# Optimization experiments

Measured on AMD Instinct MI355X. Metric: run time of the kernel, lower is better.

The kernel has to match this reference:

```python
import jax, jax.numpy as jnp
import numpy as np

# Loihi neuron constants (from netParams['neuron'])
VTH_MANT = 80.0
THETA = VTH_MANT * 64.0          # Loihi threshold = vThMant * 2**6
I_DECAY = 1024.0                 # current decay (of 4096)
V_DECAY = 128.0                  # voltage decay (of 4096)
REF_DELAY = 1.0                  # refractory steps after a spike
W_SCALE = 64.0                   # Loihi weighted-input scaling (2**6)
TAU_RHO = 1.0
POOL_W = 1.1 * VTH_MANT          # slayer pool synapse weight (one spike fires output)


@jax.custom_vjp
def spike(v):
    return (v >= THETA).astype(v.dtype)

def _spike_fwd(v):
    return spike(v), v

def _spike_bwd(v, g):
    # SLAYER surrogate gradient: exponential pdf around threshold
    return (g * jnp.exp(-jnp.abs(v - THETA) / (TAU_RHO * THETA)) / THETA,)

spike.defvjp(_spike_fwd, _spike_bwd)


def loihi_dynamics(wsum):
    """CUBA Loihi LIF over time-leading weighted input wsum: [T, ...] -> spikes [T, ...]."""
    i_dec = (4096.0 - I_DECAY) / 4096.0
    v_dec = (4096.0 - V_DECAY) / 4096.0

    def step(carry, x):
        u, v, ref = carry
        u = i_dec * u + W_SCALE * x                    # synaptic current
        v = jnp.where(ref > 0, 0.0, v_dec * v + u)     # membrane, clamped in refractory
        s = spike(v)
        v = v * (1.0 - s)                              # reset on spike
        ref = jnp.where(s > 0, REF_DELAY, jnp.maximum(ref - 1.0, 0.0))
        return (u, v, ref), s

    z = jnp.zeros_like(wsum[0])
    _, s = jax.lax.scan(step, (z, z, z), wsum)
    return s


def delay_shift(s):
    # slayer.delayShift(spike, 1): shift spike train by 1 timestep (time-leading axis)
    return jnp.concatenate([jnp.zeros_like(s[:1]), s[:-1]], axis=0)


def conv2d_t(x, w, pad):
    # x: [T, B, C, H, W]; fold T into batch for the spatial conv
    T, B, C, H, W = x.shape
    y = jax.lax.conv_general_dilated(
        x.reshape(T * B, C, H, W), w, (1, 1), [(pad, pad), (pad, pad)],
        dimension_numbers=('NCHW', 'OIHW', 'NCHW'))
    return y.reshape(T, B, y.shape[1], y.shape[2], y.shape[3])


def sum_pool(x, k):
    # slayer pool: per-channel sum pooling with fixed synaptic weight POOL_W
    y = jax.lax.reduce_window(x, 0.0, jax.lax.add,
                              (1, 1, 1, k, k), (1, 1, 1, k, k), 'VALID')
    return POOL_W * y


def setup_inputs() -> dict:
    key = jax.random.key(0)
    ks = jax.random.split(key, 6)
    B, C, H, W, T = 48, 4, 26, 26, 128
    # Bernoulli(0.1) spike trains
    spike_input = (jax.random.uniform(ks[0], (B, C, H, W, T)) < 0.1).astype(jnp.float32)
    w_conv1 = jax.random.normal(ks[1], (8, 4, 5, 5), jnp.float32) * 4.0
    w_conv2 = jax.random.normal(ks[2], (16, 8, 3, 3), jnp.float32) * 4.0
    w_conv3 = jax.random.normal(ks[3], (32, 16, 3, 3), jnp.float32) * 4.0
    w_fc1 = jax.random.normal(ks[4], (512, 3 * 3 * 32), jnp.float32) * 4.0
    w_fc2 = jax.random.normal(ks[5], (2, 512), jnp.float32) * 4.0
    return {"spike_input": spike_input, "w_conv1": w_conv1, "w_conv2": w_conv2,
            "w_conv3": w_conv3, "w_fc1": w_fc1, "w_fc2": w_fc2}


def reference(spike_input, w_conv1, w_conv2, w_conv3, w_fc1, w_fc2):
    x = jnp.transpose(spike_input, (4, 0, 1, 2, 3))  # [T, B, C, H, W]

    def block(x, w, pad):
        s = delay_shift(loihi_dynamics(conv2d_t(x, w, pad)))
        s = delay_shift(loihi_dynamics(sum_pool(s, 2)))
        return s  # dropout is identity in eval

    x = block(x, w_conv1, 1)   # 26 -> 24 -> 12
    x = block(x, w_conv2, 1)   # 12 -> 12 -> 6
    x = block(x, w_conv3, 1)   # 6 -> 6 -> 3
    T, B = x.shape[0], x.shape[1]
    x = x.reshape(T, B, -1)    # [T, B, 32*3*3] (C,H,W flatten order matches torch view)
    s = delay_shift(loihi_dynamics(jnp.einsum('tbi,oi->tbo', x, w_fc1)))
    s = delay_shift(loihi_dynamics(jnp.einsum('tbi,oi->tbo', s, w_fc2)))
    return jnp.transpose(s, (1, 2, 0))  # [B, 2, T]
```

## Files before the change

### kernel.cpp

```cpp
#include <hip/hip_runtime.h>


#define THETA 5120.0f

typedef __attribute__((ext_vector_type(8))) short bfrag;
typedef __attribute__((ext_vector_type(4))) float ffrag;

__device__ __forceinline__ float dyn_step(float x, float& u, float& v, float& r) {
#pragma clang fp contract(off)
    u = 0.75f * u + 64.0f * x;
    float vn = 0.96875f * v + u;
    vn = (r > 0.0f) ? 0.0f : vn;
    float s;
    if (vn >= THETA) { s = 1.0f; v = 0.0f; r = 1.0f; }
    else             { s = 0.0f; v = vn; r = fmaxf(r - 1.0f, 0.0f); }
    return s;
}

__device__ __forceinline__ float dpp_add_xor1(float x) {
    int y = __builtin_amdgcn_update_dpp(0, __float_as_int(x), 0xB1, 0xF, 0xF, true);
    return x + __int_as_float(y);
}
__device__ __forceinline__ float dpp_add_xor2(float x) {
    int y = __builtin_amdgcn_update_dpp(0, __float_as_int(x), 0x4E, 0xF, 0xF, true);
    return x + __int_as_float(y);
}

__device__ __forceinline__ unsigned int compress4(unsigned long long x) {
    x &= 0x1111111111111111ull;
    x = (x | (x >> 3))  & 0x0303030303030303ull;
    x = (x | (x >> 6))  & 0x000F000F000F000Full;
    x = (x | (x >> 12)) & 0x000000FF000000FFull;
    x = (x | (x >> 24)) & 0xFFFFull;
    return (unsigned int)x;
}

__device__ __forceinline__ unsigned short f2bf(float f) {
    unsigned int u = __float_as_uint(f);
    unsigned int r = (u + 0x7FFFu + ((u >> 16) & 1u)) >> 16;
    return (unsigned short)r;
}
__device__ __forceinline__ float bf2f(unsigned short b) {
    return __uint_as_float(((unsigned int)b) << 16);
}

__device__ __forceinline__ float f4_elem(float4 v, int j) {
    return (j == 0) ? v.x : (j == 1) ? v.y : (j == 2) ? v.z : v.w;
}

__global__ __launch_bounds__(256) void k_masks(const float* __restrict__ in,
                                               const float* __restrict__ wfc1,
                                               uint2* __restrict__ xb,
                                               unsigned short* __restrict__ wb) {
    if (blockIdx.x >= 624) {
        int gid = (blockIdx.x - 624) * 256 + threadIdx.x;
        int o = gid / 288, k = gid % 288;
        float w = wfc1[gid];
        unsigned short b0 = f2bf(w);
        float r1 = w - bf2f(b0);
        unsigned short b1 = f2bf(r1);
        float r2 = r1 - bf2f(b1);
        unsigned short b2 = f2bf(r2);
        size_t ob = (size_t)o * 864 + k;
        wb[ob]       = b0;
        wb[ob + 288] = b1;
        wb[ob + 576] = b2;
        return;
    }
    int wv = blockIdx.x * 4 + (threadIdx.x >> 6);
    int lane = threadIdx.x & 63;
    int y = wv % 26; int r = wv / 26;
    int pr = r & 1; int b = r >> 1;
    int ch = lane >> 5;
    int x = lane & 31;
    int act = x < 26;
    int xc = act ? x : 25;
    const float4* src = (const float4*)(in + (size_t)(((b * 4 + pr * 2 + ch) * 26 + y) * 26 + xc) * 128);
    uint2* dst = xb + ((size_t)b * 2 + pr) * 28 + (y + 1);
    if (y == 0) {
        uint2* pp = xb + ((size_t)b * 2 + pr) * 28;
        uint2 z = make_uint2(0u, 0u);
#pragma unroll
        for (int h = 0; h < 2; ++h) {
            int t = h * 64 + lane;
            pp[(size_t)t * 2688] = z;
            pp[(size_t)t * 2688 + 27] = z;
        }
    }
    for (int t4 = 0; t4 < 32; ++t4) {
        float4 f = src[t4];
#pragma unroll
        for (int k = 0; k < 4; ++k) {
            float fv = f4_elem(f, k);
            unsigned long long bal = __ballot(act && (fv != 0.0f));
            if (lane == 0) {
                unsigned int lo = ((unsigned int)bal & 0x03FFFFFFu) << 1;
                unsigned int hi = ((unsigned int)(bal >> 32) & 0x03FFFFFFu) << 1;
                dst[(size_t)(t4 * 4 + k) * 2688] = make_uint2(lo, hi);
            }
        }
    }
}

__global__ __launch_bounds__(576) void k_wsum1(const uint2* __restrict__ xb,
                                               const float* __restrict__ w1,
                                               float* __restrict__ ws) {
    __shared__ float wsh[400];
    __shared__ ffrag tbl4[660];
    int tid = threadIdx.x;
    int H = blockIdx.x & 1;
    int bid = blockIdx.x >> 1;
    int tch = bid & 15;
    int b = bid >> 4;
    float* wsH = ws + (size_t)H * 14155776;
    if (tid < 400) wsh[tid] = w1[H * 400 + tid];
    __syncthreads();
    for (int e = tid; e < 660; e += 576) {
        int ch = e / 165;
        int rem = e % 165;
        int ky = rem / 33;
        int idx = rem % 33;
        ffrag val = {0.f, 0.f, 0.f, 0.f};
#pragma unroll
        for (int oc4 = 0; oc4 < 4; ++oc4) {
            float a = 0.f;
#pragma unroll
            for (int k = 0; k < 5; ++k)
                a += ((idx >> k) & 1) ? wsh[oc4 * 100 + ch * 25 + ky * 5 + k] : 0.f;
            val[oc4] = a;
        }
        tbl4[(ch * 5 + ky) * 33 + idx] = val;
    }
    __syncthreads();
    int q = tid >> 2, s = tid & 3;
    int ox = (q % 12) * 2 + (s & 1);
    int oy = (q / 12) * 2 + (s >> 1);
    int t0 = tch * 8;
    ffrag acc[8];
#pragma unroll
    for (int j = 0; j < 8; ++j) {
        int t = t0 + j;
        const uint2* rp = xb + ((size_t)t * 48 + b) * 56 + oy;
        ffrag a = {0.f, 0.f, 0.f, 0.f};
#pragma unroll
        for (int ky = 0; ky < 5; ++ky) {
            uint2 r0 = rp[ky];
            uint2 r1 = rp[28 + ky];
            a += tbl4[ky * 33 + (int)((r0.x >> ox) & 31u)];
            a += tbl4[(5 + ky) * 33 + (int)((r0.y >> ox) & 31u)];
            a += tbl4[(10 + ky) * 33 + (int)((r1.x >> ox) & 31u)];
            a += tbl4[(15 + ky) * 33 + (int)((r1.y >> ox) & 31u)];
        }
        acc[j] = a;
    }
    size_t tilebase = (size_t)(t0 >> 4) * 1769472 + (t0 & 15);
#pragma unroll
    for (int oc4 = 0; oc4 < 4; ++oc4) {
        float* wp = wsH + tilebase + (size_t)((b * 4 + oc4) * 576 + tid) * 16;
        *(float4*)(wp)     = make_float4(acc[0][oc4], acc[1][oc4], acc[2][oc4], acc[3][oc4]);
        *(float4*)(wp + 4) = make_float4(acc[4][oc4], acc[5][oc4], acc[6][oc4], acc[7][oc4]);
    }
}

__global__ __launch_bounds__(576) void k_scan1(const float* __restrict__ ws,
                                               unsigned short* __restrict__ pb16) {
    __shared__ unsigned short sh[9 * 128];
    int tid = threadIdx.x;
    int sub = tid >> 6, lane = tid & 63;
    int blk = blockIdx.x;
    int H = (blk >= 192) ? 1 : 0;
    int ibl = blk - H * 192;
    int b = ibl >> 2, ocl = ibl & 3;
    int oc = H * 4 + ocl;
    const float* bp = ws + (size_t)H * 14155776 + (size_t)((ibl * 9 + sub) * 64 + lane) * 16;
    float u = 0.f, v = 0.f, rf = 0.f;
    float pu = 0.f, pv = 0.f, prf = 0.f;
    float sp = 0.f;
    unsigned int mb[4];
    float4 cur[4], nxt[4];
#pragma unroll
    for (int i = 0; i < 4; ++i) cur[i] = *(const float4*)(bp + i * 4);
    for (int tb = 0; tb < 8; ++tb) {
        if (tb < 7) {
            const float* np = bp + (size_t)(tb + 1) * 1769472;
#pragma unroll
            for (int i = 0; i < 4; ++i) nxt[i] = *(const float4*)(np + i * 4);
        }
#pragma unroll
        for (int j = 0; j < 16; ++j) {
            int t = tb * 16 + j;
            float w = f4_elem(cur[j >> 2], j & 3);
            float cnt = dpp_add_xor2(dpp_add_xor1(sp));
            float ps = dyn_step(88.0f * cnt, pu, pv, prf);
            unsigned long long bal = __ballot(((lane & 3) == 0) && (ps > 0.5f));
            unsigned int m = compress4(bal);
            int sl = (t >> 1) & 3;
            mb[sl] = (t & 1) ? (mb[sl] | (m << 16)) : m;
            if ((t & 7) == 7 && lane == 0)
                *(uint4*)(&sh[sub * 128 + (t & ~7)]) = make_uint4(mb[0], mb[1], mb[2], mb[3]);
            sp = dyn_step(w, u, v, rf);
        }
        if (tb < 7) {
#pragma unroll
            for (int i = 0; i < 4; ++i) cur[i] = nxt[i];
        }
    }
    __syncthreads();
    for (int idx = tid; idx < 1536; idx += 576) {
        int t = idx / 12, y = idx % 12;
        int Q0 = y * 12;
        int w0 = Q0 >> 4, off = Q0 & 15;
        unsigned int v0 = sh[w0 * 128 + t];
        unsigned int v1 = (off > 4) ? (unsigned int)sh[(w0 + 1) * 128 + t] : 0u;
        unsigned int m = ((v0 >> off) | (v1 << (16 - off))) & 0xFFFu;
        size_t rowb = (size_t)(t * 48 + b) * 14;
        pb16[(rowb + y + 1) * 8 + oc] = (unsigned short)(m << 1);
        if (y == 0)  pb16[rowb * 8 + oc] = 0;
        if (y == 11) pb16[(rowb + 13) * 8 + oc] = 0;
    }
}

__global__ __launch_bounds__(576) void k_wsum2(const unsigned short* __restrict__ pb16,
                                               const float* __restrict__ w2,
                                               float* __restrict__ ws) {
    __shared__ float wsh[288];
    __shared__ ffrag tbl4[852];
    int tid = threadIdx.x;
    int tch = blockIdx.x & 3;
    int r = blockIdx.x >> 2;
    int ocg = r & 3; int b = r >> 2;
    if (tid < 288) wsh[tid] = w2[(ocg * 4 + tid / 72) * 72 + (tid % 72)];
    __syncthreads();
    for (int e = tid; e < 852; e += 576) {
        int pr = e / 213;
        int rem = e % 213;
        int ky = rem / 71;
        int idx = rem % 71;
        int lo = idx % 9, hi = idx / 9;
        ffrag val = {0.f, 0.f, 0.f, 0.f};
#pragma unroll
        for (int oc4 = 0; oc4 < 4; ++oc4) {
            float a = 0.f;
#pragma unroll
            for (int k = 0; k < 3; ++k)
                a += ((lo >> k) & 1) ? wsh[oc4 * 72 + (2 * pr) * 9 + ky * 3 + k] : 0.f;
#pragma unroll
            for (int k = 0; k < 3; ++k)
                a += ((hi >> k) & 1) ? wsh[oc4 * 72 + (2 * pr + 1) * 9 + ky * 3 + k] : 0.f;
            val[oc4] = a;
        }
        tbl4[(pr * 3 + ky) * 71 + idx] = val;
    }
    __syncthreads();
    int tq = tid / 144;
    int pix = tid % 144;
    int q = pix >> 2, s = pix & 3;
    int ox = (q % 6) * 2 + (s & 1);
    int oy = (q / 6) * 2 + (s >> 1);
    int t0 = tch * 32 + tq * 8;
    ffrag acc[8];
#pragma unroll
    for (int j = 0; j < 8; ++j) {
        int t = t0 + j;
        ffrag a = {0.f, 0.f, 0.f, 0.f};
        if (t > 0) {
            const uint4* rp = (const uint4*)(pb16 + (((size_t)(t - 1) * 48 + b) * 14 + oy) * 8);
#pragma unroll
            for (int ky = 0; ky < 3; ++ky) {
                uint4 row = rp[ky];
                unsigned int wd[4] = {row.x, row.y, row.z, row.w};
#pragma unroll
                for (int pr = 0; pr < 4; ++pr) {
                    unsigned int lo = (wd[pr] >> ox) & 7u;
                    unsigned int hi = (wd[pr] >> (16 + ox)) & 7u;
                    a += tbl4[(pr * 3 + ky) * 71 + (int)(lo + 9u * hi)];
                }
            }
        }
        acc[j] = a;
    }
    size_t tilebase = (size_t)(t0 >> 4) * 1769472 + (t0 & 15);
#pragma unroll
    for (int oc4 = 0; oc4 < 4; ++oc4) {
        int neuron = (b * 16 + ocg * 4 + oc4) * 144 + pix;
        float* wp = ws + tilebase + (size_t)neuron * 16;
        *(float4*)(wp)     = make_float4(acc[0][oc4], acc[1][oc4], acc[2][oc4], acc[3][oc4]);
        *(float4*)(wp + 4) = make_float4(acc[4][oc4], acc[5][oc4], acc[6][oc4], acc[7][oc4]);
    }
}

__global__ __launch_bounds__(576) void k_scan2(const float* __restrict__ ws,
                                               unsigned short* __restrict__ pb2) {
    __shared__ unsigned short sh[9 * 128];
    int tid = threadIdx.x;
    int wloc = tid >> 6, lane = tid & 63;
    int g4 = blockIdx.x;
    const float* bp = ws + (size_t)(g4 * 576 + tid) * 16;
    float u = 0.f, v = 0.f, rf = 0.f;
    float pu = 0.f, pv = 0.f, prf = 0.f;
    float sp = 0.f;
    unsigned int mb[4];
    float4 cur[4], nxt[4];
#pragma unroll
    for (int i = 0; i < 4; ++i) cur[i] = *(const float4*)(bp + i * 4);
    for (int tb = 0; tb < 8; ++tb) {
        if (tb < 7) {
            const float* np = bp + (size_t)(tb + 1) * 1769472;
#pragma unroll
            for (int i = 0; i < 4; ++i) nxt[i] = *(const float4*)(np + i * 4);
        }
#pragma unroll
        for (int j = 0; j < 16; ++j) {
            int t = tb * 16 + j;
            float w = f4_elem(cur[j >> 2], j & 3);
            float cnt = dpp_add_xor2(dpp_add_xor1(sp));
            float ps = dyn_step(88.0f * cnt, pu, pv, prf);
            unsigned long long bal = __ballot(((lane & 3) == 0) && (ps > 0.5f));
            unsigned int m = compress4(bal);
            int sl = (t >> 1) & 3;
            mb[sl] = (t & 1) ? (mb[sl] | (m << 16)) : m;
            if ((t & 7) == 7 && lane == 0)
                *(uint4*)(&sh[wloc * 128 + (t & ~7)]) = make_uint4(mb[0], mb[1], mb[2], mb[3]);
            sp = dyn_step(w, u, v, rf);
        }
        if (tb < 7) {
#pragma unroll
            for (int i = 0; i < 4; ++i) cur[i] = nxt[i];
        }
    }
    __syncthreads();
    for (int idx = tid; idx < 3072; idx += 576) {
        int t = idx / 24;
        int r2 = idx % 24;
        int lI = r2 / 6, y = r2 % 6;
        int img = g4 * 4 + lI;
        int b = img >> 4, oc = img & 15;
        int Q0 = lI * 36 + y * 6;
        int w0 = Q0 >> 4, off = Q0 & 15;
        unsigned int v0 = sh[w0 * 128 + t];
        unsigned int v1 = (off > 10) ? (unsigned int)sh[(w0 + 1) * 128 + t] : 0u;
        unsigned int m = ((v0 >> off) | (v1 << (16 - off))) & 0x3Fu;
        size_t rowb = (size_t)(t * 48 + b) * 8;
        pb2[(rowb + y + 1) * 16 + oc] = (unsigned short)(m << 1);
        if (y == 0) pb2[rowb * 16 + oc] = 0;
        if (y == 5) pb2[(rowb + 7) * 16 + oc] = 0;
    }
}

__global__ __launch_bounds__(576) void k_wsum3(const unsigned short* __restrict__ pb2,
                                               const float* __restrict__ w3,
                                               float* __restrict__ ws) {
    __shared__ float wsh[576];
    __shared__ ffrag tbl4[1704];
    int tid = threadIdx.x;
    int tch = blockIdx.x & 7;
    int gb = blockIdx.x >> 3;
    int ocg = gb / 12, bg = gb % 12;
    wsh[tid] = w3[(ocg * 4 + tid / 144) * 144 + (tid % 144)];
    __syncthreads();
    for (int e = tid; e < 1536; e += 576) {
        int pr = e / 192;
        int ky = (e / 64) % 3;
        int i = e & 63;
        int lo = i & 7, hi = i >> 3;
        ffrag val = {0.f, 0.f, 0.f, 0.f};
#pragma unroll
        for (int oc4 = 0; oc4 < 4; ++oc4) {
            float a = 0.f;
#pragma unroll
            for (int k = 0; k < 3; ++k)
                a += ((lo >> k) & 1) ? wsh[oc4 * 144 + (2 * pr) * 9 + ky * 3 + k] : 0.f;
#pragma unroll
            for (int k = 0; k < 3; ++k)
                a += ((hi >> k) & 1) ? wsh[oc4 * 144 + (2 * pr + 1) * 9 + ky * 3 + k] : 0.f;
            val[oc4] = a;
        }
        tbl4[(pr * 3 + ky) * 71 + lo + 9 * hi] = val;
    }
    __syncthreads();
    int tq = tid & 3;
    int r = tid >> 2;
    int pix = r % 36;
    int bsel = r / 36;
    int q = pix >> 2, s = pix & 3;
    int ox = (q % 3) * 2 + (s & 1);
    int oy = (q / 3) * 2 + (s >> 1);
    int b = bg * 4 + bsel;
    int t0 = tch * 16 + tq * 4;
    ffrag acc[4];
#pragma unroll
    for (int j = 0; j < 4; ++j) {
        int t = t0 + j;
        ffrag a = {0.f, 0.f, 0.f, 0.f};
        if (t > 0) {
            const uint4* rp = (const uint4*)(pb2 + (((size_t)(t - 1) * 48 + b) * 8 + oy) * 16);
#pragma unroll
            for (int ky = 0; ky < 3; ++ky) {
                uint4 rA = rp[ky * 2];
                uint4 rB = rp[ky * 2 + 1];
                unsigned int wd[8] = {rA.x, rA.y, rA.z, rA.w, rB.x, rB.y, rB.z, rB.w};
#pragma unroll
                for (int pr = 0; pr < 8; ++pr) {
                    unsigned int lo = (wd[pr] >> ox) & 7u;
                    unsigned int hi = (wd[pr] >> (16 + ox)) & 7u;
                    a += tbl4[(pr * 3 + ky) * 71 + (int)(lo + 9u * hi)];
                }
            }
        }
        acc[j] = a;
    }
    size_t base = (size_t)tch * 884736;
#pragma unroll
    for (int oc4 = 0; oc4 < 4; ++oc4) {
        int neuron = (b * 32 + ocg * 4 + oc4) * 36 + pix;
        float* wp = ws + base + (size_t)neuron * 16 + tq * 4;
        *(float4*)(wp) = make_float4(acc[0][oc4], acc[1][oc4], acc[2][oc4], acc[3][oc4]);
    }
}

__global__ __launch_bounds__(256) void k_scan3(const float* __restrict__ ws,
                                               unsigned short* __restrict__ a3) {
    __shared__ unsigned short sh[4 * 128];
    int tid = threadIdx.x;
    int wloc = tid >> 6, lane = tid & 63;
    int wv = blockIdx.x * 4 + wloc;
    const float* bp = ws + (size_t)(wv * 64 + lane) * 16;
    float u = 0.f, v = 0.f, rf = 0.f;
    float pu = 0.f, pv = 0.f, prf = 0.f;
    float sp = 0.f;
    unsigned int mb[4];
    float4 cur[4], nxt[4];
#pragma unroll
    for (int i = 0; i < 4; ++i) cur[i] = *(const float4*)(bp + i * 4);
    for (int tb = 0; tb < 8; ++tb) {
        if (tb < 7) {
            const float* np = bp + (size_t)(tb + 1) * 884736;
#pragma unroll
            for (int i = 0; i < 4; ++i) nxt[i] = *(const float4*)(np + i * 4);
        }
#pragma unroll
        for (int j = 0; j < 16; ++j) {
            int t = tb * 16 + j;
            float w = f4_elem(cur[j >> 2], j & 3);
            float cnt = dpp_add_xor2(dpp_add_xor1(sp));
            float ps = dyn_step(88.0f * cnt, pu, pv, prf);
            unsigned long long bal = __ballot(((lane & 3) == 0) && (ps > 0.5f));
            unsigned int m = compress4(bal);
            int sl = (t >> 1) & 3;
            mb[sl] = (t & 1) ? (mb[sl] | (m << 16)) : m;
            if ((t & 7) == 7 && lane == 0)
                *(uint4*)(&sh[wloc * 128 + (t & ~7)]) = make_uint4(mb[0], mb[1], mb[2], mb[3]);
            sp = dyn_step(w, u, v, rf);
        }
        if (tb < 7) {
#pragma unroll
            for (int i = 0; i < 4; ++i) cur[i] = nxt[i];
        }
    }
    __syncthreads();
    int G0 = blockIdx.x * 64;
    int g = tid & 63, tq = tid >> 6;
    if (tq == 0) a3[G0 + g] = 0;
    for (int t = tq; t < 127; t += 4) {
        unsigned int bit = ((unsigned int)sh[(g >> 4) * 128 + t] >> (g & 15)) & 1u;
        a3[(size_t)(t + 1) * 13824 + G0 + g] = bit ? 0x3F80 : 0;
    }
}

__global__ __launch_bounds__(256) void k_fc1mm(const unsigned short* __restrict__ a3,
                                               const unsigned short* __restrict__ wb,
                                               float* __restrict__ wsf1) {
    __shared__ unsigned short Bs[16 * 872];
    int tid = threadIdx.x;
    int nt = blockIdx.x & 31;
    int mc = blockIdx.x >> 5;
    int n0 = nt * 16;
    for (int idx = tid; idx < 13824; idx += 256) {
        int n = idx / 864;
        int kp = idx % 864;
        Bs[n * 872 + kp] = wb[(size_t)(n0 + n) * 864 + kp];
    }
    __syncthreads();
    int wave = tid >> 6;
    int lane = tid & 63;
    int ln = lane & 15, quad = lane >> 4;
#pragma unroll
    for (int i = 0; i < 4; ++i) {
        int m0 = (mc * 16 + wave * 4 + i) * 16;
        const unsigned short* arow = a3 + (size_t)(m0 + ln) * 288 + quad * 8;
        ffrag acc = {0.f, 0.f, 0.f, 0.f};
#pragma unroll
        for (int kb = 0; kb < 9; ++kb) {
            bfrag av = *(const bfrag*)(arow + kb * 32);
#pragma unroll
            for (int c = 0; c < 3; ++c) {
                bfrag bv = *(const bfrag*)(&Bs[ln * 872 + c * 288 + kb * 32 + quad * 8]);
                acc = __builtin_amdgcn_mfma_f32_16x16x32_bf16(av, bv, acc, 0, 0, 0);
            }
        }
        float* wout = wsf1 + (size_t)(m0 + quad * 4) * 512 + n0 + ln;
        wout[0] = acc[0];
        wout[512] = acc[1];
        wout[1024] = acc[2];
        wout[1536] = acc[3];
    }
}

__global__ __launch_bounds__(256) void k_fc1s(const float* __restrict__ wsf1,
                                              float* __restrict__ f1f) {
    int tid = blockIdx.x * 256 + threadIdx.x;
    float u = 0.f, v = 0.f, rf = 0.f;
    float wbuf[16];
#pragma unroll
    for (int i = 0; i < 16; ++i) wbuf[i] = wsf1[(size_t)i * 24576 + tid];
    for (int tb = 0; tb < 128; tb += 16) {
#pragma unroll
        for (int j = 0; j < 16; ++j) {
            int t = tb + j;
            float w = wbuf[j];
            if (t + 16 < 128) wbuf[j] = wsf1[(size_t)(t + 16) * 24576 + tid];
            float s = dyn_step(w, u, v, rf);
            f1f[(size_t)t * 24576 + tid] = s;
        }
    }
}

__global__ __launch_bounds__(256) void k_fc2w(const float* __restrict__ f1f,
                                              const float* __restrict__ wfc2,
                                              float* __restrict__ wsf2) {
    int wv = blockIdx.x * 4 + (threadIdx.x >> 6);
    int lane = threadIdx.x & 63;
    int b = wv % 48, t = wv / 48;
    int o = lane & 1, kq = lane >> 1;
    float acc = 0.f;
    if (t > 0) {
        const float* wp = wfc2 + o * 512 + kq * 16;
        const float* sp = f1f + (size_t)(t - 1) * 24576 + b * 512 + kq * 16;
#pragma unroll
        for (int i = 0; i < 16; ++i) acc += wp[i] * sp[i];
    }
#pragma unroll
    for (int m = 2; m < 64; m <<= 1) acc += __shfl_xor(acc, m, 64);
    if (lane < 2) wsf2[(size_t)t * 96 + b * 2 + o] = acc;
}

__global__ __launch_bounds__(128) void k_fc2s(const float* __restrict__ wsf2,
                                              float* __restrict__ out) {
    int tid = threadIdx.x;
    if (tid >= 96) return;
    float* ob = out + tid * 128;
    ob[0] = 0.0f;
    float u = 0.f, v = 0.f, rf = 0.f;
    float wbuf[8];
#pragma unroll
    for (int i = 0; i < 8; ++i) wbuf[i] = wsf2[(size_t)i * 96 + tid];
    for (int tb = 0; tb < 128; tb += 8) {
#pragma unroll
        for (int j = 0; j < 8; ++j) {
            int t = tb + j;
            float w = wbuf[j];
            if (t + 8 < 128) wbuf[j] = wsf2[(size_t)(t + 8) * 96 + tid];
            float s = dyn_step(w, u, v, rf);
            if (t < 127) ob[t + 1] = s;
        }
    }
}

extern "C" void kernel_launch(void* const* d_in, const int* in_sizes, int n_in,
                              void* d_out, int out_size, void* d_ws, size_t ws_size,
                              hipStream_t stream) {
    const float* in   = (const float*)d_in[0];
    const float* w1   = (const float*)d_in[1];
    const float* w2   = (const float*)d_in[2];
    const float* w3   = (const float*)d_in[3];
    const float* wfc1 = (const float*)d_in[4];
    const float* wfc2 = (const float*)d_in[5];
    float* out = (float*)d_out;
    char* ws = (char*)d_ws;

    float*          slab = (float*)(ws);
    uint2*          xb   = (uint2*)(ws + 113246208);
    unsigned short* pb16 = (unsigned short*)(ws + 115998720);
    unsigned short* pb2  = (unsigned short*)(ws + 117374976);
    float*          f1f  = (float*)(ws + 118947840);
    unsigned short* a3   = (unsigned short*)(ws + 131530752);
    unsigned short* wb   = (unsigned short*)(ws + 135069696);
    float*          wsf1 = (float*)(ws);
    float*          wsf2 = (float*)(ws + 16777216);

    k_masks   <<<1200, 256, 0, stream>>>(in, wfc1, xb, wb);
    k_wsum1   <<<1536, 576, 0, stream>>>(xb, w1, slab);
    k_scan1   <<<384, 576, 0, stream>>>(slab, pb16);
    k_wsum2   <<<768, 576, 0, stream>>>(pb16, w2, slab);
    k_scan2   <<<192, 576, 0, stream>>>(slab, pb2);
    k_wsum3   <<<768, 576, 0, stream>>>(pb2, w3, slab);
    k_scan3   <<<216, 256, 0, stream>>>(slab, a3);
    k_fc1mm   <<<768, 256, 0, stream>>>(a3, wb, wsf1);
    k_fc1s    <<<96, 256, 0, stream>>>(wsf1, f1f);
    k_fc2w    <<<1536, 256, 0, stream>>>(f1f, wfc2, wsf2);
    k_fc2s    <<<1, 128, 0, stream>>>(wsf2, out);
}
```

Before: 371.2 us.

## Fuse fc1 scan, fc2 matmul and fc2 scan into one per-batch kernel

Replaces the three tail kernels (fc1 LIF scan, fc2 weighted sum, fc2 LIF scan) with a single kernel, one block per batch element. fc1 spikes are packed into ballot bitmasks in shared memory rather than written to global memory as floats, and fc2 sums only the weights of set bits. This drops two launches and the global round trip of the fc1 spike tensor. The cost is parallelism: the fc1 scan now runs on 48 blocks of 512 threads instead of 96 blocks of 256, and the fc2 scan is done serially by two threads per block.

```diff
diff --git a/kernel.cpp b/kernel.cpp
--- a/kernel.cpp
+++ b/kernel.cpp
@@ -506,61 +506,66 @@
     }
 }
 
-__global__ __launch_bounds__(256) void k_fc1s(const float* __restrict__ wsf1,
-                                              float* __restrict__ f1f) {
-    int tid = blockIdx.x * 256 + threadIdx.x;
-    float u = 0.f, v = 0.f, rf = 0.f;
-    float wbuf[16];
-#pragma unroll
-    for (int i = 0; i < 16; ++i) wbuf[i] = wsf1[(size_t)i * 24576 + tid];
-    for (int tb = 0; tb < 128; tb += 16) {
-#pragma unroll
-        for (int j = 0; j < 16; ++j) {
-            int t = tb + j;
-            float w = wbuf[j];
-            if (t + 16 < 128) wbuf[j] = wsf1[(size_t)(t + 16) * 24576 + tid];
-            float s = dyn_step(w, u, v, rf);
-            f1f[(size_t)t * 24576 + tid] = s;
-        }
-    }
-}
-
-__global__ __launch_bounds__(256) void k_fc2w(const float* __restrict__ f1f,
-                                              const float* __restrict__ wfc2,
-                                              float* __restrict__ wsf2) {
-    int wv = blockIdx.x * 4 + (threadIdx.x >> 6);
-    int lane = threadIdx.x & 63;
-    int b = wv % 48, t = wv / 48;
-    int o = lane & 1, kq = lane >> 1;
-    float acc = 0.f;
-    if (t > 0) {
-        const float* wp = wfc2 + o * 512 + kq * 16;
-        const float* sp = f1f + (size_t)(t - 1) * 24576 + b * 512 + kq * 16;
-#pragma unroll
-        for (int i = 0; i < 16; ++i) acc += wp[i] * sp[i];
-    }
-#pragma unroll
-    for (int m = 2; m < 64; m <<= 1) acc += __shfl_xor(acc, m, 64);
-    if (lane < 2) wsf2[(size_t)t * 96 + b * 2 + o] = acc;
-}
-
-__global__ __launch_bounds__(128) void k_fc2s(const float* __restrict__ wsf2,
-                                              float* __restrict__ out) {
-    int tid = threadIdx.x;
-    if (tid >= 96) return;
-    float* ob = out + tid * 128;
-    ob[0] = 0.0f;
-    float u = 0.f, v = 0.f, rf = 0.f;
-    float wbuf[8];
-#pragma unroll
-    for (int i = 0; i < 8; ++i) wbuf[i] = wsf2[(size_t)i * 96 + tid];
-    for (int tb = 0; tb < 128; tb += 8) {
-#pragma unroll
-        for (int j = 0; j < 8; ++j) {
-            int t = tb + j;
-            float w = wbuf[j];
-            if (t + 8 < 128) wbuf[j] = wsf2[(size_t)(t + 8) * 96 + tid];
-            float s = dyn_step(w, u, v, rf);
+__global__ __launch_bounds__(512) void k_fctail(const float* __restrict__ wsf1,
+                                                const float* __restrict__ wfc2,
+                                                float* __restrict__ out) {
+    __shared__ unsigned int shb[128 * 16];
+    __shared__ float wsh[1024];
+    __shared__ float sums[256];
+    int tid = threadIdx.x;
+    int b = blockIdx.x;
+    for (int e = tid; e < 1024; e += 512) wsh[e] = wfc2[e];
+    int wv = tid >> 6, lane = tid & 63;
+    {
+        const float* wp0 = wsf1 + b * 512 + tid;
+        float u = 0.f, v = 0.f, rf = 0.f;
+        float wbuf[16];
+#pragma unroll
+        for (int i = 0; i < 16; ++i) wbuf[i] = wp0[(size_t)i * 24576];
+        for (int tb = 0; tb < 128; tb += 16) {
+#pragma unroll
+            for (int j = 0; j < 16; ++j) {
+                int t = tb + j;
+                float w = wbuf[j];
+                if (t + 16 < 128) wbuf[j] = wp0[(size_t)(t + 16) * 24576];
+                float s = dyn_step(w, u, v, rf);
+                unsigned long long bal = __ballot(s > 0.5f);
+                if (lane == 0)  shb[t * 16 + wv * 2]     = (unsigned int)bal;
+                if (lane == 32) shb[t * 16 + wv * 2 + 1] = (unsigned int)(bal >> 32);
+            }
+        }
+    }
+    __syncthreads();
+    if (tid < 256) {
+        int t = tid >> 1, o = tid & 1;
+        float p[32];
+        if (t > 0) {
+#pragma unroll
+            for (int kq = 0; kq < 32; ++kq) {
+                unsigned int bw = shb[(t - 1) * 16 + (kq >> 1)] >> ((kq & 1) * 16);
+                float a = 0.f;
+#pragma unroll
+                for (int i = 0; i < 16; ++i)
+                    if ((bw >> i) & 1u) a += wsh[o * 512 + kq * 16 + i];
+                p[kq] = a;
+            }
+        } else {
+#pragma unroll
+            for (int kq = 0; kq < 32; ++kq) p[kq] = 0.f;
+        }
+#pragma unroll
+        for (int m = 1; m < 32; m <<= 1)
+            for (int kq = 0; kq < 32; kq += 2 * m)
+                p[kq] = p[kq] + p[kq + m];
+        sums[t * 2 + o] = p[0];
+    }
+    __syncthreads();
+    if (tid < 2) {
+        float* ob = out + (b * 2 + tid) * 128;
+        ob[0] = 0.0f;
+        float u = 0.f, v = 0.f, rf = 0.f;
+        for (int t = 0; t < 128; ++t) {
+            float s = dyn_step(sums[t * 2 + tid], u, v, rf);
             if (t < 127) ob[t + 1] = s;
         }
     }
@@ -582,11 +587,9 @@
     uint2*          xb   = (uint2*)(ws + 113246208);
     unsigned short* pb16 = (unsigned short*)(ws + 115998720);
     unsigned short* pb2  = (unsigned short*)(ws + 117374976);
-    float*          f1f  = (float*)(ws + 118947840);
     unsigned short* a3   = (unsigned short*)(ws + 131530752);
     unsigned short* wb   = (unsigned short*)(ws + 135069696);
     float*          wsf1 = (float*)(ws);
-    float*          wsf2 = (float*)(ws + 16777216);
 
     k_masks   <<<1200, 256, 0, stream>>>(in, wfc1, xb, wb);
     k_wsum1   <<<1536, 576, 0, stream>>>(xb, w1, slab);
@@ -596,7 +599,5 @@
     k_wsum3   <<<768, 576, 0, stream>>>(pb2, w3, slab);
     k_scan3   <<<216, 256, 0, stream>>>(slab, a3);
     k_fc1mm   <<<768, 256, 0, stream>>>(a3, wb, wsf1);
-    k_fc1s    <<<96, 256, 0, stream>>>(wsf1, f1f);
-    k_fc2w    <<<1536, 256, 0, stream>>>(f1f, wfc2, wsf2);
-    k_fc2s    <<<1, 128, 0, stream>>>(wsf2, out);
-}
+    k_fctail  <<<48, 512, 0, stream>>>(wsf1, wfc2, out);
+}
```

Result: slower. 423.1 us (+14.0%).
